# Kernel optimization log

Measured on AMD Instinct MI355X. Metric: run time of the kernel, lower is better.

The kernel has to match this reference:

```python
import jax, jax.numpy as jnp
from jax import lax
import numpy as np

S = 4          # tile_length
T = 16         # tile_size = S**2
K = 7          # length_inter_tile
NI = 49        # num_inter = K**2
CH_DE = 7      # design channels
EPS = 0.01
NEG = 0.01     # LeakyReLU default slope


def _conv(x, w, b, stride, pad):
    y = lax.conv_general_dilated(x, w, (stride, stride), [(pad, pad), (pad, pad)],
                                 dimension_numbers=('NCHW', 'OIHW', 'NCHW'))
    return y + b[None, :, None, None]


def _lrelu(x):
    return jax.nn.leaky_relu(x, NEG)


def _unfold(x, k=K):
    # torch F.unfold(x, k, padding=k//2): (B,C,H,W) -> (B, C*k*k, H*W), (c,i,j) ordering
    pad = k // 2
    B, C, H, W = x.shape
    xp = jnp.pad(x, ((0, 0), (0, 0), (pad, pad), (pad, pad)))
    cols = jnp.stack([xp[:, :, i:i + H, j:j + W] for i in range(k) for j in range(k)], axis=2)
    return cols.reshape(B, C * k * k, H * W)


def setup_inputs():
    key = jax.random.key(0)
    ks = jax.random.split(key, 16)
    B, H, W = 1, 48, 48
    CIN = 10; CF = 100; CW = 1024
    FINAL = T * T * NI  # 12544
    HALF = FINAL // 2   # 6272
    def w_init(k, shape, fan_in):
        return jax.random.normal(k, shape, jnp.float32) * np.float32(np.sqrt(2.0 / fan_in))
    return {
        'input': jax.random.normal(ks[0], (B, T, CIN, H, W), jnp.float32),
        'design': jax.random.normal(ks[1], (B, T, CH_DE, H, W), jnp.float32),
        'fw0': w_init(ks[2], (CF, CIN, 3, 3), CIN * 9),
        'fb0': jnp.zeros((CF,), jnp.float32),
        'fw_rest': w_init(ks[3], (13, CF, CF, 3, 3), CF * 9),
        'fb_rest': jnp.zeros((13, CF), jnp.float32),
        'ww0': w_init(ks[4], (CW, CF, S, S), CF * S * S),
        'wb0': jnp.zeros((CW,), jnp.float32),
        'ww_mid': w_init(ks[5], (3, CW, CW, 3, 3), CW * 9),
        'wb_mid': jnp.zeros((3, CW), jnp.float32),
        'ww1': w_init(ks[6], (HALF, CW, 1, 1), CW),
        'wb1': jnp.zeros((HALF,), jnp.float32),
        'ww2': w_init(ks[7], (FINAL, HALF, 1, 1), HALF),
        'wb2': jnp.zeros((FINAL,), jnp.float32),
    }


def reference(input, design, fw0, fb0, fw_rest, fb_rest, ww0, wb0, ww_mid, wb_mid, ww1, wb1, ww2, wb2):
    B, _, CIN, H, W = input.shape
    hw = H * W
    # domain: (B*hw, T, CH_DE)
    domain = design.transpose(0, 3, 4, 1, 2).reshape(B * hw, T, CH_DE)
    # X from unfolded design: (B*hw*NI, T, CH_DE)
    u = _unfold(design.reshape(B, T * CH_DE, H, W))
    X = u.reshape(B, T * CH_DE, NI, hw).transpose(0, 3, 2, 1).reshape(B * hw * NI, T, CH_DE)
    # make_full_res_img: stack tile (s*i + j) -> spatial offset (i, j)
    full = input.reshape(B, S, S, CIN, H, W).transpose(0, 3, 4, 1, 5, 2).reshape(B, CIN, H * S, W * S)
    # feature network: 14 conv3x3 + LeakyReLU at full res
    f = _lrelu(_conv(full, fw0, fb0, 1, 1))
    for i in range(fw_rest.shape[0]):
        f = _lrelu(_conv(f, fw_rest[i], fb_rest[i], 1, 1))
    g = _lrelu(_conv(f, ww0, wb0, S, 0))
    for i in range(ww_mid.shape[0]):
        g = _lrelu(_conv(g, ww_mid[i], wb_mid[i], 1, 1))
    g = _lrelu(_conv(g, ww1, wb1, 1, 0))
    Wmap = jnp.tanh(_conv(g, ww2, wb2, 1, 0))  # (B, NI*T*T, H, W)
    Wm = Wmap.reshape(B, NI, T, T, H, W).transpose(0, 4, 5, 1, 2, 3).reshape(B * hw * NI, T, T)
    Wm = Wm @ Wm.transpose(0, 2, 1) + jnp.eye(T, dtype=Wm.dtype)
    # normal equations
    XTW = X.transpose(0, 2, 1) @ Wm                                  # (N, CH_DE, T)
    A = (XTW @ X).reshape(B * hw, NI, CH_DE, CH_DE).sum(axis=1)
    A = A + EPS * jnp.eye(CH_DE, dtype=A.dtype)
    # all 3 color channels at once (same math as per-channel loop)
    Yu = _unfold(input[:, :, :3].reshape(B, T * 3, H, W))            # (B, T*3*NI, hw)
    Y = Yu.reshape(B, T, 3, NI, hw).transpose(0, 4, 3, 1, 2).reshape(B * hw * NI, T, 3)
    Bv = (XTW @ Y).reshape(B * hw, NI, CH_DE, 3).sum(axis=1)         # (B*hw, CH_DE, 3)
    para = jnp.linalg.solve(A, Bv)                                   # (B*hw, CH_DE, 3)
    out = (domain @ para).reshape(B, H, W, T, 3).transpose(0, 3, 4, 1, 2)
    return out
```

## Files before the change

### kernel.cpp

```cpp
#include <hip/hip_runtime.h>
#include <math.h>

#define LRELU(v) ((v) > 0.f ? (v) : 0.01f * (v))

typedef __attribute__((ext_vector_type(8))) short bf8v;
typedef __attribute__((ext_vector_type(4))) float f4v;

static __device__ __forceinline__ unsigned short f2b(float f) {
    unsigned int u = __float_as_uint(f);
    unsigned int r = (u + 0x7fffu + ((u >> 16) & 1u)) >> 16;
    return (unsigned short)r;
}

static __device__ __forceinline__ void gload16(const unsigned short* g, unsigned short* l) {
    __builtin_amdgcn_global_load_lds(
        (__attribute__((address_space(1))) void*)(g),
        (__attribute__((address_space(3))) void*)(l), 16, 0, 0);
}

__global__ __launch_bounds__(256) void k_build_full(const float* __restrict__ in,
                                                    unsigned short* __restrict__ full0p) {
    int idx = blockIdx.x * 256 + threadIdx.x;
    if (idx >= 368640) return;
    int c = idx % 10, pix = idx / 10;
    int X = pix % 192, Y = pix / 192;
    int t = (Y & 3) * 4 + (X & 3);
    int h = Y >> 2, w = X >> 2;
    int pp = (Y + 1) * 194 + (X + 1);
    full0p[(size_t)pp * 16 + c] = f2b(in[(((t * 10 + c) * 48) + h) * 48 + w]);
}

template <int C, int CP, int Q>
__global__ __launch_bounds__(256) void k_wcvt(const float* __restrict__ src,
                                              unsigned short* __restrict__ dst,
                                              int Mv, int Kp) {
    int m = blockIdx.x;
    for (int kp = threadIdx.x; kp < Kp; kp += 256) {
        int qq = kp / CP, c = kp - qq * CP;
        float v = 0.f;
        if (m < Mv && c < C && qq < Q)
            v = src[((size_t)m * C + c) * Q + qq];
        dst[(size_t)m * Kp + kp] = f2b(v);
    }
}

__global__ __launch_bounds__(256) void k_cvt_flat(const float* __restrict__ src,
                                                  unsigned short* __restrict__ dst,
                                                  size_t n) {
    size_t i = ((size_t)blockIdx.x * 256 + threadIdx.x) * 4;
    if (i >= n) return;
    float4 v = *(const float4*)(src + i);
    ushort4 o;
    o.x = f2b(v.x); o.y = f2b(v.y); o.z = f2b(v.z); o.w = f2b(v.w);
    *(ushort4*)(dst + i) = o;
}

__global__ __launch_bounds__(256) void k_im2col4(const unsigned short* __restrict__ src,
                                                 unsigned short* __restrict__ dst) {
    int p = blockIdx.x;
    int x = p % 48, y = p / 48;
    for (int kp = threadIdx.x; kp < 1600; kp += 256) {
        int qq = kp / 100, c = kp - qq * 100;
        int yy = y * 4 + (qq >> 2), xx = x * 4 + (qq & 3);
        dst[(size_t)p * 1600 + kp] = src[(size_t)((yy + 1) * 194 + (xx + 1)) * 104 + c];
    }
}

template <int ACT, int OF32, int REMAP, int SWZ>
__global__ __launch_bounds__(256) void k_gemm(
    const unsigned short* __restrict__ A, const unsigned short* __restrict__ Bt,
    const float* __restrict__ bias, void* __restrict__ outv,
    int K, int Mv, int ldout) {
    __shared__ __align__(16) unsigned short As[128 * 32];
    __shared__ __align__(16) unsigned short Bs[128 * 32];
    const int tid = threadIdx.x;
    const int lane = tid & 63;
    const int w = tid >> 6;
    const int wm = w >> 1, wn = w & 1;
    const int q = lane >> 4, ln = lane & 15;
    int bx = blockIdx.x, by = blockIdx.y;
    if (SWZ) {
        int gx = gridDim.x;
        int nwg = gx * gridDim.y;
        int lin = by * gx + bx;
        int qq = nwg >> 3, rr = nwg & 7;
        int xcd = lin & 7, idx = lin >> 3;
        int wg = (xcd < rr ? xcd * (qq + 1) : rr * (qq + 1) + (xcd - rr) * qq) + idx;
        bx = wg % gx; by = wg / gx;
    }
    const int m0 = by * 128, n0 = bx * 128;

    f4v acc[4][4];
#pragma unroll
    for (int i = 0; i < 4; ++i)
#pragma unroll
        for (int j = 0; j < 4; ++j) acc[i][j] = (f4v){0.f, 0.f, 0.f, 0.f};

    const int br0 = tid >> 2, bk0 = (tid & 3) << 3;
    const unsigned short* pA0 = A + (size_t)(m0 + br0) * K + bk0;
    const unsigned short* pA1 = pA0 + (size_t)64 * K;
    const unsigned short* pB0 = Bt + (size_t)(n0 + br0) * K + bk0;
    const unsigned short* pB1 = pB0 + (size_t)64 * K;
    unsigned short* lA0 = As + tid * 8;
    unsigned short* lA1 = As + 2048 + tid * 8;
    unsigned short* lB0 = Bs + tid * 8;
    unsigned short* lB1 = Bs + 2048 + tid * 8;
    const unsigned short* Ap2 = &As[(wm * 64 + ln) * 32 + q * 8];
    const unsigned short* Bp2 = &Bs[(wn * 64 + ln) * 32 + q * 8];

    for (int k0 = 0; k0 < K; k0 += 32) {
        gload16(pA0 + k0, lA0);
        gload16(pA1 + k0, lA1);
        gload16(pB0 + k0, lB0);
        gload16(pB1 + k0, lB1);
        __syncthreads();
        bf8v af[4], bfv[4];
#pragma unroll
        for (int i = 0; i < 4; ++i) af[i] = *(const bf8v*)(Ap2 + i * 512);
#pragma unroll
        for (int j = 0; j < 4; ++j) bfv[j] = *(const bf8v*)(Bp2 + j * 512);
#pragma unroll
        for (int i = 0; i < 4; ++i)
#pragma unroll
            for (int j = 0; j < 4; ++j)
                acc[i][j] = __builtin_amdgcn_mfma_f32_16x16x32_bf16(af[i], bfv[j], acc[i][j], 0, 0, 0);
        __syncthreads();
    }

    float* tb = ((float*)As) + w * 288;
#pragma unroll
    for (int i = 0; i < 4; ++i) {
        const int mbase = m0 + wm * 64 + i * 16;
        float bi[4];
#pragma unroll
        for (int r = 0; r < 4; ++r) {
            int mm = mbase + q * 4 + r;
            bi[r] = (mm < Mv) ? bias[mm] : 0.f;
        }
#pragma unroll
        for (int j = 0; j < 4; ++j) {
            const int nbase = n0 + wn * 64 + j * 16;
#pragma unroll
            for (int r = 0; r < 4; ++r) {
                float v = acc[i][j][r] + bi[r];
                v = ACT ? tanhf(v) : LRELU(v);
                tb[ln * 17 + q * 4 + r] = v;
            }
#pragma unroll
            for (int r = 0; r < 4; ++r) {
                float v = tb[(q * 4 + r) * 17 + ln];
                int n = nbase + q * 4 + r;
                int m = mbase + ln;
                if (m < Mv) {
                    if (REMAP == 3) {
                        int y = n / 48, x = n - y * 48;
                        size_t np = (size_t)((y + 1) * 50 + x + 1);
                        ((unsigned short*)outv)[np * (size_t)ldout + m] = f2b(v);
                    } else {
                        if (OF32) ((float*)outv)[(size_t)n * ldout + m] = v;
                        else ((unsigned short*)outv)[(size_t)n * ldout + m] = f2b(v);
                    }
                }
            }
        }
    }
}

template <int TAPK, int CST, int SH, int REMAP>
__global__ __launch_bounds__(256) void k_cgemm(
    const unsigned short* __restrict__ A, const unsigned short* __restrict__ Bt,
    const float* __restrict__ bias, unsigned short* __restrict__ outp,
    int Mv, int ldout) {
    __shared__ __align__(16) unsigned short As[128 * 32];
    __shared__ __align__(16) unsigned short Bs[128 * 32];
    const int tid = threadIdx.x;
    const int lane = tid & 63;
    const int w = tid >> 6;
    const int wm = w >> 1, wn = w & 1;
    const int q = lane >> 4, ln = lane & 15;
    const int m0 = blockIdx.y * 128, n0 = blockIdx.x * 128;
    const int KA = 9 * TAPK;

    f4v acc[4][4];
#pragma unroll
    for (int i = 0; i < 4; ++i)
#pragma unroll
        for (int j = 0; j < 4; ++j) acc[i][j] = (f4v){0.f, 0.f, 0.f, 0.f};

    const int br0 = tid >> 2, bk0 = (tid & 3) << 3;
    const unsigned short* pA0 = A + (size_t)(m0 + br0) * KA + bk0;
    const unsigned short* pA1 = pA0 + (size_t)64 * KA;
    unsigned short* lA0 = As + tid * 8;
    unsigned short* lA1 = As + 2048 + tid * 8;
    unsigned short* lB0 = Bs + tid * 8;
    unsigned short* lB1 = Bs + 2048 + tid * 8;
    const unsigned short* Ap2 = &As[(wm * 64 + ln) * 32 + q * 8];
    const unsigned short* Bp2 = &Bs[(wn * 64 + ln) * 32 + q * 8];

#pragma unroll
    for (int tap = 0; tap < 9; ++tap) {
        const int sh = (tap / 3 - 1) * SH + (tap % 3 - 1);
        const unsigned short* pB0 = Bt + (long)(n0 + br0 + sh) * CST + bk0;
        const unsigned short* pB1 = pB0 + (long)64 * CST;
        const int kab = tap * TAPK;
        for (int kk = 0; kk < TAPK; kk += 32) {
            gload16(pA0 + kab + kk, lA0);
            gload16(pA1 + kab + kk, lA1);
            gload16(pB0 + kk, lB0);
            gload16(pB1 + kk, lB1);
            __syncthreads();
            bf8v af[4], bfv[4];
#pragma unroll
            for (int i = 0; i < 4; ++i) af[i] = *(const bf8v*)(Ap2 + i * 512);
#pragma unroll
            for (int j = 0; j < 4; ++j) bfv[j] = *(const bf8v*)(Bp2 + j * 512);
#pragma unroll
            for (int i = 0; i < 4; ++i)
#pragma unroll
                for (int j = 0; j < 4; ++j)
                    acc[i][j] = __builtin_amdgcn_mfma_f32_16x16x32_bf16(af[i], bfv[j], acc[i][j], 0, 0, 0);
            __syncthreads();
        }
    }

    float* tb = ((float*)As) + w * 288;
#pragma unroll
    for (int i = 0; i < 4; ++i) {
        const int mbase = m0 + wm * 64 + i * 16;
        float bi[4];
#pragma unroll
        for (int r = 0; r < 4; ++r) {
            int mm = mbase + q * 4 + r;
            bi[r] = (mm < Mv) ? bias[mm] : 0.f;
        }
#pragma unroll
        for (int j = 0; j < 4; ++j) {
            const int nbase = n0 + wn * 64 + j * 16;
#pragma unroll
            for (int r = 0; r < 4; ++r) {
                float v = acc[i][j][r] + bi[r];
                v = LRELU(v);
                tb[ln * 17 + q * 4 + r] = v;
            }
#pragma unroll
            for (int r = 0; r < 4; ++r) {
                float v = tb[(q * 4 + r) * 17 + ln];
                int n = nbase + q * 4 + r;
                int m = mbase + ln;
                if (m < Mv) {
                    if (REMAP == 1) {
                        int y = n / 194, x = n - y * 194;
                        bool z = (n >= 37636) || y == 0 || y >= 193 || x == 0 || x >= 193;
                        outp[(size_t)n * ldout + m] = f2b(z ? 0.f : v);
                    } else if (REMAP == 2) {
                        int y = n / 50, x = n - y * 50;
                        bool z = (n >= 2500) || y == 0 || y >= 49 || x == 0 || x >= 49;
                        outp[(size_t)n * ldout + m] = f2b(z ? 0.f : v);
                    } else if (REMAP == 4) {
                        int y = n / 50, x = n - y * 50;
                        if (n < 2500 && y >= 1 && y <= 48 && x >= 1 && x <= 48)
                            outp[(size_t)((y - 1) * 48 + (x - 1)) * ldout + m] = f2b(v);
                    }
                }
            }
        }
    }
}

template <int ACT, int OF32, int AF32>
__global__ __launch_bounds__(256) void k_gemm_f32a(
    const void* __restrict__ Ain, const unsigned short* __restrict__ Bt,
    const float* __restrict__ bias, void* __restrict__ outv,
    int K, int Mv, int ldout) {
    __shared__ __align__(16) unsigned short As[128 * 40];
    __shared__ __align__(16) unsigned short Bs[128 * 40];
    const int tid = threadIdx.x;
    const int lane = tid & 63;
    const int w = tid >> 6;
    const int wm = w >> 1, wn = w & 1;
    const int q = lane >> 4, ln = lane & 15;
    const int m0 = blockIdx.y * 128, n0 = blockIdx.x * 128;

    f4v acc[4][4];
#pragma unroll
    for (int i = 0; i < 4; ++i)
#pragma unroll
        for (int j = 0; j < 4; ++j) acc[i][j] = (f4v){0.f, 0.f, 0.f, 0.f};

    const int br0 = tid >> 2, bk0 = (tid & 3) << 3;
    const int br1 = br0 + 64;
    const int bl0 = br0 * 40 + bk0, bl1 = br1 * 40 + bk0;
    const unsigned short* pB0 = Bt + (size_t)(n0 + br0) * K + bk0;
    const unsigned short* pB1 = Bt + (size_t)(n0 + br1) * K + bk0;

    const unsigned short* Ab = (const unsigned short*)Ain;
    const float* Af = (const float*)Ain;
    const unsigned short* pA0 = Ab + (size_t)(m0 + br0) * K + bk0;
    const unsigned short* pA1 = Ab + (size_t)(m0 + br1) * K + bk0;
    const int fr = tid >> 3, fk = (tid & 7) << 2;
    const float* pF = Af + (size_t)(m0 + fr) * K + fk;

    for (int k0 = 0; k0 < K; k0 += 32) {
        if (AF32) {
#pragma unroll
            for (int jj = 0; jj < 4; ++jj) {
                float4 v = *(const float4*)(pF + (size_t)jj * 32 * K + k0);
                unsigned int lo = ((unsigned)f2b(v.y) << 16) | f2b(v.x);
                unsigned int hi = ((unsigned)f2b(v.w) << 16) | f2b(v.z);
                *(uint2*)&As[(fr + jj * 32) * 40 + fk] = make_uint2(lo, hi);
            }
        } else {
            uint4 a0 = *(const uint4*)(pA0 + k0);
            uint4 a1 = *(const uint4*)(pA1 + k0);
            *(uint4*)&As[bl0] = a0;
            *(uint4*)&As[bl1] = a1;
        }
        uint4 b0 = *(const uint4*)(pB0 + k0);
        uint4 b1 = *(const uint4*)(pB1 + k0);
        *(uint4*)&Bs[bl0] = b0;
        *(uint4*)&Bs[bl1] = b1;
        __syncthreads();
        const unsigned short* Ap2 = &As[(wm * 64 + ln) * 40 + q * 8];
        const unsigned short* Bp2 = &Bs[(wn * 64 + ln) * 40 + q * 8];
        bf8v af[4], bfv[4];
#pragma unroll
        for (int i = 0; i < 4; ++i) af[i] = *(const bf8v*)(Ap2 + i * 640);
#pragma unroll
        for (int j = 0; j < 4; ++j) bfv[j] = *(const bf8v*)(Bp2 + j * 640);
#pragma unroll
        for (int i = 0; i < 4; ++i)
#pragma unroll
            for (int j = 0; j < 4; ++j)
                acc[i][j] = __builtin_amdgcn_mfma_f32_16x16x32_bf16(af[i], bfv[j], acc[i][j], 0, 0, 0);
        __syncthreads();
    }

    float* tb = ((float*)As) + w * 288;
#pragma unroll
    for (int i = 0; i < 4; ++i) {
        const int mbase = m0 + wm * 64 + i * 16;
        float bi[4];
#pragma unroll
        for (int r = 0; r < 4; ++r) {
            int mm = mbase + q * 4 + r;
            bi[r] = (mm < Mv) ? bias[mm] : 0.f;
        }
#pragma unroll
        for (int j = 0; j < 4; ++j) {
            const int nbase = n0 + wn * 64 + j * 16;
#pragma unroll
            for (int r = 0; r < 4; ++r) {
                float v = acc[i][j][r] + bi[r];
                v = ACT ? tanhf(v) : LRELU(v);
                tb[ln * 17 + q * 4 + r] = v;
            }
#pragma unroll
            for (int r = 0; r < 4; ++r) {
                float v = tb[(q * 4 + r) * 17 + ln];
                size_t n = nbase + q * 4 + r;
                int m = mbase + ln;
                if (m < Mv) {
                    if (OF32) ((float*)outv)[n * (size_t)ldout + m] = v;
                    else ((unsigned short*)outv)[n * (size_t)ldout + m] = f2b(v);
                }
            }
        }
    }
}

__global__ __launch_bounds__(256) void k_solve(const float* __restrict__ WmT,
                                               const float* __restrict__ design,
                                               const float* __restrict__ input,
                                               float* __restrict__ out) {
    const int p = blockIdx.x;
    const int h = p / 48, wpx = p % 48;
    const int tid = threadIdx.x;
    __shared__ float Msh[16 * 17];
    __shared__ float Gsh[16 * 17];
    __shared__ float Xsh[16 * 8];
    __shared__ float Ysh[16 * 4];
    __shared__ float XTWsh[7 * 17];
    __shared__ float Aacc[49];
    __shared__ float Bacc[21];
    __shared__ float parash[21];

    if (tid < 49) Aacc[tid] = 0.f;
    if (tid >= 64 && tid < 85) Bacc[tid - 64] = 0.f;
    __syncthreads();

    const float* wrow = WmT + (size_t)p * 12544;
    for (int ni = 0; ni < 49; ++ni) {
        {
            int t1 = tid >> 4, t2 = tid & 15;
            Msh[t1 * 17 + t2] = wrow[ni * 256 + tid];
        }
        int sy = h + ni / 7 - 3, sx = wpx + ni % 7 - 3;
        bool inb = (sy >= 0 && sy < 48 && sx >= 0 && sx < 48);
        if (tid < 112) {
            int t = tid / 7, c = tid - t * 7;
            Xsh[t * 8 + c] = inb ? design[(size_t)(t * 7 + c) * 2304 + sy * 48 + sx] : 0.f;
        } else if (tid >= 128 && tid < 176) {
            int l = tid - 128;
            int t = l / 3, r = l - t * 3;
            Ysh[t * 4 + r] = inb ? input[(size_t)(t * 10 + r) * 2304 + sy * 48 + sx] : 0.f;
        }
        __syncthreads();
        {
            int t1 = tid >> 4, t2 = tid & 15;
            float s = (t1 == t2) ? 1.f : 0.f;
#pragma unroll
            for (int k = 0; k < 16; ++k) s += Msh[t1 * 17 + k] * Msh[t2 * 17 + k];
            Gsh[t1 * 17 + t2] = s;
        }
        __syncthreads();
        if (tid < 112) {
            int c = tid >> 4, t2 = tid & 15;
            float s = 0.f;
#pragma unroll
            for (int t1 = 0; t1 < 16; ++t1) s += Xsh[t1 * 8 + c] * Gsh[t1 * 17 + t2];
            XTWsh[c * 17 + t2] = s;
        }
        __syncthreads();
        if (tid < 49) {
            int c1 = tid / 7, c2 = tid - c1 * 7;
            float s = 0.f;
#pragma unroll
            for (int t = 0; t < 16; ++t) s += XTWsh[c1 * 17 + t] * Xsh[t * 8 + c2];
            Aacc[tid] += s;
        } else if (tid >= 64 && tid < 85) {
            int l = tid - 64;
            int c = l / 3, r = l - c * 3;
            float s = 0.f;
#pragma unroll
            for (int t = 0; t < 16; ++t) s += XTWsh[c * 17 + t] * Ysh[t * 4 + r];
            Bacc[l] += s;
        }
        __syncthreads();
    }

    if (tid == 0) {
        float Mg[7][10];
#pragma unroll
        for (int i = 0; i < 7; ++i) {
#pragma unroll
            for (int j = 0; j < 7; ++j) Mg[i][j] = Aacc[i * 7 + j] + ((i == j) ? 0.01f : 0.f);
#pragma unroll
            for (int r = 0; r < 3; ++r) Mg[i][7 + r] = Bacc[i * 3 + r];
        }
#pragma unroll
        for (int kk = 0; kk < 7; ++kk) {
            float inv = 1.f / Mg[kk][kk];
#pragma unroll
            for (int j = 0; j < 10; ++j) Mg[kk][j] *= inv;
#pragma unroll
            for (int i = 0; i < 7; ++i) {
                if (i == kk) continue;
                float f = Mg[i][kk];
#pragma unroll
                for (int j = 0; j < 10; ++j) Mg[i][j] -= f * Mg[kk][j];
            }
        }
#pragma unroll
        for (int c = 0; c < 7; ++c)
#pragma unroll
            for (int r = 0; r < 3; ++r) parash[c * 3 + r] = Mg[c][7 + r];
    }
    __syncthreads();

    if (tid < 48) {
        int t = tid / 3, r = tid - t * 3;
        float s = 0.f;
#pragma unroll
        for (int c = 0; c < 7; ++c)
            s += design[(size_t)(t * 7 + c) * 2304 + p] * parash[c * 3 + r];
        out[(size_t)tid * 2304 + p] = s;
    }
}

extern "C" void kernel_launch(void* const* d_in, const int* in_sizes, int n_in,
                              void* d_out, int out_size, void* d_ws, size_t ws_size,
                              hipStream_t stream) {
    const float* input   = (const float*)d_in[0];
    const float* design  = (const float*)d_in[1];
    const float* fw0     = (const float*)d_in[2];
    const float* fb0     = (const float*)d_in[3];
    const float* fw_rest = (const float*)d_in[4];
    const float* fb_rest = (const float*)d_in[5];
    const float* ww0     = (const float*)d_in[6];
    const float* wb0     = (const float*)d_in[7];
    const float* ww_mid  = (const float*)d_in[8];
    const float* wb_mid  = (const float*)d_in[9];
    const float* ww1     = (const float*)d_in[10];
    const float* wb1     = (const float*)d_in[11];
    const float* ww2     = (const float*)d_in[12];
    const float* wb2     = (const float*)d_in[13];
    float* out = (float*)d_out;
    float* ws = (float*)d_ws;

    float* WmT = ws;
    unsigned short* full0p = (unsigned short*)(ws + 40000);
    unsigned short* actPA  = (unsigned short*)(ws + 350000);
    unsigned short* actPB  = (unsigned short*)(ws + 2330000);
    unsigned short* fw0c   = (unsigned short*)(ws + 4310000);
    unsigned short* fwrb   = (unsigned short*)(ws + 4330000);
    unsigned short* ww0b   = (unsigned short*)(ws + 5290000);
    unsigned short* col4   = (unsigned short*)(ws + 6110000);
    unsigned short* gPA    = (unsigned short*)(ws + 7960000);
    unsigned short* gPB    = (unsigned short*)(ws + 9340000);
    unsigned short* wmb    = (unsigned short*)(ws + 10720000);
    unsigned short* gcmp   = (unsigned short*)(ws + 15440000);
    unsigned short* g1     = (unsigned short*)(ws + 28901376);
    unsigned short* ww1b   = (unsigned short*)(ws + 36126720);
    const size_t WS_BASE_F = 39337984ull;
    unsigned short* ww2b   = (unsigned short*)(ws + WS_BASE_F);

    hipMemsetAsync(full0p, 0, (size_t)37956 * 16 * 2, stream);
    hipMemsetAsync(actPA, 0, (size_t)37956 * 104 * 2, stream);
    hipMemsetAsync(actPB, 0, (size_t)37956 * 104 * 2, stream);
    hipMemsetAsync(gPA, 0, (size_t)2688 * 1024 * 2, stream);
    hipMemsetAsync(gPB, 0, (size_t)2688 * 1024 * 2, stream);

    k_wcvt<10, 32, 9><<<128, 256, 0, stream>>>(fw0, fw0c, 100, 288);
    for (int i = 0; i < 13; ++i)
        k_wcvt<100, 128, 9><<<128, 256, 0, stream>>>(fw_rest + (size_t)i * 90000,
                                                     fwrb + (size_t)i * 147456, 100, 1152);
    k_wcvt<100, 100, 16><<<1024, 256, 0, stream>>>(ww0, ww0b, 1024, 1600);
    k_wcvt<1024, 1024, 1><<<6272, 256, 0, stream>>>(ww1, ww1b, 6272, 1024);

    k_build_full<<<1440, 256, 0, stream>>>(input, full0p);
    k_cgemm<32, 16, 194, 1><<<dim3(295, 1), 256, 0, stream>>>(fw0c, full0p, fb0, actPA, 100, 104);
    unsigned short* src = actPA;
    unsigned short* dst = actPB;
    for (int i = 0; i < 13; ++i) {
        k_cgemm<128, 104, 194, 1><<<dim3(295, 1), 256, 0, stream>>>(
            fwrb + (size_t)i * 147456, src, fb_rest + i * 100, dst, 100, 104);
        unsigned short* t = src; src = dst; dst = t;
    }

    k_im2col4<<<2304, 256, 0, stream>>>(src, col4);
    k_gemm<0, 0, 3, 0><<<dim3(18, 8), 256, 0, stream>>>(ww0b, col4, wb0, gPA, 1600, 1024, 1024);

    k_wcvt<1024, 1024, 9><<<1024, 256, 0, stream>>>(ww_mid, wmb, 1024, 9216);
    k_cgemm<1024, 1024, 50, 2><<<dim3(20, 8), 256, 0, stream>>>(wmb, gPA, wb_mid, gPB, 1024, 1024);
    k_wcvt<1024, 1024, 9><<<1024, 256, 0, stream>>>(ww_mid + (size_t)9437184, wmb, 1024, 9216);
    k_cgemm<1024, 1024, 50, 2><<<dim3(20, 8), 256, 0, stream>>>(wmb, gPB, wb_mid + 1024, gPA, 1024, 1024);
    k_wcvt<1024, 1024, 9><<<1024, 256, 0, stream>>>(ww_mid + (size_t)2 * 9437184, wmb, 1024, 9216);
    k_cgemm<1024, 1024, 50, 4><<<dim3(20, 8), 256, 0, stream>>>(wmb, gPA, wb_mid + 2048, gcmp, 1024, 1024);

    k_gemm<0, 0, 0, 1><<<dim3(18, 49), 256, 0, stream>>>(ww1b, gcmp, wb1, g1, 1024, 6272, 6272);

    const size_t haveF = ws_size / 4;
    if (haveF >= WS_BASE_F + 39337984ull) {
        k_cvt_flat<<<76832, 256, 0, stream>>>(ww2, ww2b, (size_t)12544 * 6272);
        k_gemm<1, 1, 0, 1><<<dim3(18, 98), 256, 0, stream>>>(ww2b, g1, wb2, WmT, 6272, 12544, 12544);
    } else if (haveF >= WS_BASE_F + 19668992ull) {
        for (int c = 0; c < 2; ++c) {
            k_cvt_flat<<<38416, 256, 0, stream>>>(ww2 + (size_t)c * 6272 * 6272, ww2b,
                                                  (size_t)6272 * 6272);
            k_gemm<1, 1, 0, 1><<<dim3(18, 49), 256, 0, stream>>>(
                ww2b, g1, wb2 + c * 6272, WmT + (size_t)c * 6272, 6272, 6272, 12544);
        }
    } else {
        k_gemm_f32a<1, 1, 1><<<dim3(18, 98), 256, 0, stream>>>(ww2, g1, wb2, WmT, 6272, 12544, 12544);
    }

    k_solve<<<2304, 256, 0, stream>>>(WmT, design, input, out);
}
```

Before: 2.536 ms.

## Add 256x256 double-buffered MFMA GEMM with XCD swizzle for the 1x1 convs

Adds a 512-thread GEMM kernel with 256x256 tiles, double-buffered LDS loaded through direct global-to-LDS copies, split-K halves interleaved with barriers, setprio around the MFMA blocks, and an XCD-aware block swizzle. It replaces the 128-tile GEMM for both large 1x1 convolutions. ww1 is converted into a padded buffer so the M dimension is a multiple of 256. The goal is more data reuse per loaded tile and better L2 locality on the dominant ww2 GEMM. The cost is one block per CU and 128 KB of LDS. The intermediate chunked fallback path is removed, so a smaller workspace now drops straight to the fp32 path.

```diff
diff --git a/kernel.cpp b/kernel.cpp
--- a/kernel.cpp
+++ b/kernel.cpp
@@ -166,6 +166,151 @@
     }
 }
 
+template <int ACT, int OF32, int SWZ>
+__global__ __launch_bounds__(512, 1) void k_gemm256(
+    const unsigned short* __restrict__ A, const unsigned short* __restrict__ Bt,
+    const float* __restrict__ bias, void* __restrict__ outv,
+    int K, int Mv, int ldout) {
+    __shared__ __align__(16) unsigned short As[2][16384];
+    __shared__ __align__(16) unsigned short Bs[2][16384];
+    const int tid = threadIdx.x;
+    const int lane = tid & 63;
+    const int w = tid >> 6;
+    const int wm = w >> 2;
+    const int wn = w & 3;
+    const int q = lane >> 4, ln = lane & 15;
+
+    int bx = blockIdx.x, by = blockIdx.y;
+    if (SWZ) {
+        int gx = gridDim.x;
+        int nwg = gx * gridDim.y;
+        int lin = by * gx + bx;
+        int qq = nwg >> 3, rr = nwg & 7;
+        int xcd = lin & 7, idx = lin >> 3;
+        int wg = (xcd < rr ? xcd * (qq + 1) : rr * (qq + 1) + (xcd - rr) * qq) + idx;
+        bx = wg % gx; by = wg / gx;
+    }
+    const int m0 = by * 256, n0 = bx * 256;
+
+    f4v acc[8][4];
+#pragma unroll
+    for (int i = 0; i < 8; ++i)
+#pragma unroll
+        for (int j = 0; j < 4; ++j) acc[i][j] = (f4v){0.f, 0.f, 0.f, 0.f};
+
+    const int srow = tid >> 3;
+    const int sj = tid & 7;
+    const int sjx = sj ^ (srow & 7);
+    const unsigned short* gA = A + (size_t)(m0 + srow) * K + sjx * 8;
+    const unsigned short* gB = Bt + (size_t)(n0 + srow) * K + sjx * 8;
+    const size_t rstride = (size_t)64 * K;
+    unsigned short* lA = &As[0][0] + tid * 8;
+    unsigned short* lB = &Bs[0][0] + tid * 8;
+
+#define STAGE256(buf, t)                                               \
+    {                                                                  \
+        const unsigned short* ga_ = gA + (size_t)(t) * 64;             \
+        const unsigned short* gb_ = gB + (size_t)(t) * 64;             \
+        unsigned short* la_ = lA + (buf) * 16384;                      \
+        unsigned short* lb_ = lB + (buf) * 16384;                      \
+        _Pragma("unroll")                                              \
+        for (int r_ = 0; r_ < 4; ++r_) {                               \
+            gload16(ga_ + r_ * rstride, la_ + r_ * 4096);              \
+            gload16(gb_ + r_ * rstride, lb_ + r_ * 4096);              \
+        }                                                              \
+    }
+
+    int aoff[8], boff[4];
+#pragma unroll
+    for (int mf = 0; mf < 8; ++mf) aoff[mf] = (wm * 128 + mf * 16 + ln) * 64;
+#pragma unroll
+    for (int nf = 0; nf < 4; ++nf) boff[nf] = (wn * 64 + nf * 16 + ln) * 64;
+    const int l7 = ln & 7;
+    const int koff0 = ((0 * 4 + q) ^ l7) * 8;
+    const int koff1 = ((1 * 4 + q) ^ l7) * 8;
+
+    const int NT = K >> 6;
+    STAGE256(0, 0);
+    STAGE256(1, 1);
+    asm volatile("s_waitcnt vmcnt(8)" ::: "memory");
+    __builtin_amdgcn_sched_barrier(0);
+    __builtin_amdgcn_s_barrier();
+
+    for (int t = 0; t < NT; ++t) {
+        const int cur = t & 1;
+        const unsigned short* as = &As[cur][0];
+        const unsigned short* bs = &Bs[cur][0];
+        bf8v a0[8], b0[4], a1[8], b1[4];
+#pragma unroll
+        for (int mf = 0; mf < 8; ++mf) a0[mf] = *(const bf8v*)&as[aoff[mf] + koff0];
+#pragma unroll
+        for (int nf = 0; nf < 4; ++nf) b0[nf] = *(const bf8v*)&bs[boff[nf] + koff0];
+#pragma unroll
+        for (int mf = 0; mf < 8; ++mf) a1[mf] = *(const bf8v*)&as[aoff[mf] + koff1];
+#pragma unroll
+        for (int nf = 0; nf < 4; ++nf) b1[nf] = *(const bf8v*)&bs[boff[nf] + koff1];
+        __builtin_amdgcn_s_setprio(1);
+#pragma unroll
+        for (int mf = 0; mf < 8; ++mf)
+#pragma unroll
+            for (int nf = 0; nf < 4; ++nf)
+                acc[mf][nf] = __builtin_amdgcn_mfma_f32_16x16x32_bf16(a0[mf], b0[nf], acc[mf][nf], 0, 0, 0);
+        __builtin_amdgcn_s_setprio(0);
+        asm volatile("s_waitcnt lgkmcnt(0)" ::: "memory");
+        __builtin_amdgcn_sched_barrier(0);
+        __builtin_amdgcn_s_barrier();
+        if (t + 2 < NT) {
+            STAGE256(cur, t + 2);
+            asm volatile("s_waitcnt vmcnt(8)" ::: "memory");
+        } else {
+            asm volatile("s_waitcnt vmcnt(0)" ::: "memory");
+        }
+        __builtin_amdgcn_sched_barrier(0);
+        __builtin_amdgcn_s_barrier();
+        __builtin_amdgcn_s_setprio(1);
+#pragma unroll
+        for (int mf = 0; mf < 8; ++mf)
+#pragma unroll
+            for (int nf = 0; nf < 4; ++nf)
+                acc[mf][nf] = __builtin_amdgcn_mfma_f32_16x16x32_bf16(a1[mf], b1[nf], acc[mf][nf], 0, 0, 0);
+        __builtin_amdgcn_s_setprio(0);
+    }
+    __builtin_amdgcn_s_barrier();
+#undef STAGE256
+
+    float* tb = ((float*)&As[0][0]) + w * 288;
+#pragma unroll
+    for (int mf = 0; mf < 8; ++mf) {
+        const int mbase = m0 + wm * 128 + mf * 16;
+        float bi[4];
+#pragma unroll
+        for (int r = 0; r < 4; ++r) {
+            int mm = mbase + q * 4 + r;
+            bi[r] = (mm < Mv) ? bias[mm] : 0.f;
+        }
+#pragma unroll
+        for (int nf = 0; nf < 4; ++nf) {
+            const int nbase = n0 + wn * 64 + nf * 16;
+#pragma unroll
+            for (int r = 0; r < 4; ++r) {
+                float v = acc[mf][nf][r] + bi[r];
+                v = ACT ? tanhf(v) : LRELU(v);
+                tb[ln * 17 + q * 4 + r] = v;
+            }
+#pragma unroll
+            for (int r = 0; r < 4; ++r) {
+                float v = tb[(q * 4 + r) * 17 + ln];
+                int n = nbase + q * 4 + r;
+                int m = mbase + ln;
+                if (m < Mv) {
+                    if (OF32) ((float*)outv)[(size_t)n * ldout + m] = v;
+                    else ((unsigned short*)outv)[(size_t)n * ldout + m] = f2b(v);
+                }
+            }
+        }
+    }
+}
+
 template <int TAPK, int CST, int SH, int REMAP>
 __global__ __launch_bounds__(256) void k_cgemm(
     const unsigned short* __restrict__ A, const unsigned short* __restrict__ Bt,
@@ -513,6 +658,8 @@
     unsigned short* ww1b   = (unsigned short*)(ws + 36126720);
     const size_t WS_BASE_F = 39337984ull;
     unsigned short* ww2b   = (unsigned short*)(ws + WS_BASE_F);
+    unsigned short* ww1bp  = (unsigned short*)(ws + 59006976);
+    const size_t NEED_BIG = 59006976ull + 3276800ull;
 
     hipMemsetAsync(full0p, 0, (size_t)37956 * 16 * 2, stream);
     hipMemsetAsync(actPA, 0, (size_t)37956 * 104 * 2, stream);
@@ -520,12 +667,18 @@
     hipMemsetAsync(gPA, 0, (size_t)2688 * 1024 * 2, stream);
     hipMemsetAsync(gPB, 0, (size_t)2688 * 1024 * 2, stream);
 
+    const size_t haveF = ws_size / 4;
+    const bool big = (haveF >= NEED_BIG) && (haveF >= WS_BASE_F + 39337984ull);
+
     k_wcvt<10, 32, 9><<<128, 256, 0, stream>>>(fw0, fw0c, 100, 288);
     for (int i = 0; i < 13; ++i)
         k_wcvt<100, 128, 9><<<128, 256, 0, stream>>>(fw_rest + (size_t)i * 90000,
                                                      fwrb + (size_t)i * 147456, 100, 1152);
     k_wcvt<100, 100, 16><<<1024, 256, 0, stream>>>(ww0, ww0b, 1024, 1600);
-    k_wcvt<1024, 1024, 1><<<6272, 256, 0, stream>>>(ww1, ww1b, 6272, 1024);
+    if (big)
+        k_wcvt<1024, 1024, 1><<<6400, 256, 0, stream>>>(ww1, ww1bp, 6272, 1024);
+    else
+        k_wcvt<1024, 1024, 1><<<6272, 256, 0, stream>>>(ww1, ww1b, 6272, 1024);
 
     k_build_full<<<1440, 256, 0, stream>>>(input, full0p);
     k_cgemm<32, 16, 194, 1><<<dim3(295, 1), 256, 0, stream>>>(fw0c, full0p, fb0, actPA, 100, 104);
@@ -547,20 +700,12 @@
     k_wcvt<1024, 1024, 9><<<1024, 256, 0, stream>>>(ww_mid + (size_t)2 * 9437184, wmb, 1024, 9216);
     k_cgemm<1024, 1024, 50, 4><<<dim3(20, 8), 256, 0, stream>>>(wmb, gPA, wb_mid + 2048, gcmp, 1024, 1024);
 
-    k_gemm<0, 0, 0, 1><<<dim3(18, 49), 256, 0, stream>>>(ww1b, gcmp, wb1, g1, 1024, 6272, 6272);
-
-    const size_t haveF = ws_size / 4;
-    if (haveF >= WS_BASE_F + 39337984ull) {
+    if (big) {
+        k_gemm256<0, 0, 1><<<dim3(9, 25), 512, 0, stream>>>(ww1bp, gcmp, wb1, g1, 1024, 6272, 6272);
         k_cvt_flat<<<76832, 256, 0, stream>>>(ww2, ww2b, (size_t)12544 * 6272);
-        k_gemm<1, 1, 0, 1><<<dim3(18, 98), 256, 0, stream>>>(ww2b, g1, wb2, WmT, 6272, 12544, 12544);
-    } else if (haveF >= WS_BASE_F + 19668992ull) {
-        for (int c = 0; c < 2; ++c) {
-            k_cvt_flat<<<38416, 256, 0, stream>>>(ww2 + (size_t)c * 6272 * 6272, ww2b,
-                                                  (size_t)6272 * 6272);
-            k_gemm<1, 1, 0, 1><<<dim3(18, 49), 256, 0, stream>>>(
-                ww2b, g1, wb2 + c * 6272, WmT + (size_t)c * 6272, 6272, 6272, 12544);
-        }
+        k_gemm256<1, 1, 1><<<dim3(9, 49), 512, 0, stream>>>(ww2b, g1, wb2, WmT, 6272, 12544, 12544);
     } else {
+        k_gemm<0, 0, 0, 1><<<dim3(18, 49), 256, 0, stream>>>(ww1b, gcmp, wb1, g1, 1024, 6272, 6272);
         k_gemm_f32a<1, 1, 1><<<dim3(18, 98), 256, 0, stream>>>(ww2, g1, wb2, WmT, 6272, 12544, 12544);
     }
 
```

Result: faster. 2.362 ms (-6.9%).
